# Kernel optimization log

Measured on AMD Instinct MI355X. Metric: run time of the kernel, lower is better.

## Reference

```python
import jax, jax.numpy as jnp
import numpy as np

N = 10000      # nodes
E = 320000     # edges (before self-loops)
IN_DIM = 128
HID = 64
OUT = 32
HEADS = 8
NEG_SLOPE = 0.2  # PyG GATConv default leaky_relu slope


def gat_conv(x, W, a_src, a_dst, b, src, dst, num_nodes, heads, d):
    """One PyG-style GATConv layer (eval mode, concat=True).
    x: [N, F_in], W: [F_in, heads*d], a_src/a_dst: [heads, d], b: [heads*d]
    src/dst: [E'] int edge endpoints (self-loops already included).
    """
    h = (x @ W).reshape(num_nodes, heads, d)              # [N, H, D]
    alpha_s = jnp.sum(h * a_src, axis=-1)                 # [N, H]
    alpha_d = jnp.sum(h * a_dst, axis=-1)                 # [N, H]
    logits = jax.nn.leaky_relu(alpha_s[src] + alpha_d[dst], NEG_SLOPE)  # [E', H]
    # segment softmax over incoming edges of each destination node
    m = jax.lax.stop_gradient(
        jax.ops.segment_max(logits, dst, num_segments=num_nodes))      # [N, H]
    e = jnp.exp(logits - m[dst])                          # [E', H]
    denom = jax.ops.segment_sum(e, dst, num_segments=num_nodes)        # [N, H]
    alpha = e / denom[dst]                                # [E', H]
    out = jax.ops.segment_sum(alpha[:, :, None] * h[src], dst,
                              num_segments=num_nodes)     # [N, H, D]
    return out.reshape(num_nodes, heads * d) + b


def setup_inputs() -> dict:
    key = jax.random.key(0)
    ks = jax.random.split(key, 10)
    x = jax.random.normal(ks[0], (N, IN_DIM), jnp.float32)
    edge_index = jax.random.randint(ks[1], (2, E), 0, N, dtype=jnp.int64)
    s1 = 1.0 / np.sqrt(IN_DIM)
    W1 = jax.random.normal(ks[2], (IN_DIM, HEADS * HID), jnp.float32) * s1
    a1_src = jax.random.normal(ks[3], (HEADS, HID), jnp.float32) * 0.1
    a1_dst = jax.random.normal(ks[4], (HEADS, HID), jnp.float32) * 0.1
    b1 = jnp.zeros((HEADS * HID,), jnp.float32)
    s2 = 1.0 / np.sqrt(HEADS * HID)
    W2 = jax.random.normal(ks[5], (HEADS * HID, OUT), jnp.float32) * s2
    a2_src = jax.random.normal(ks[6], (1, OUT), jnp.float32) * 0.1
    a2_dst = jax.random.normal(ks[7], (1, OUT), jnp.float32) * 0.1
    b2 = jnp.zeros((OUT,), jnp.float32)
    return {"x": x, "edge_index": edge_index,
            "W1": W1, "a1_src": a1_src, "a1_dst": a1_dst, "b1": b1,
            "W2": W2, "a2_src": a2_src, "a2_dst": a2_dst, "b2": b2}


def reference(x, edge_index, W1, a1_src, a1_dst, b1, W2, a2_src, a2_dst, b2):
    # add self-loops (PyG GATConv default add_self_loops=True)
    loops = jnp.arange(N, dtype=edge_index.dtype)
    src = jnp.concatenate([edge_index[0], loops])
    dst = jnp.concatenate([edge_index[1], loops])
    # dropout layers are identity in eval mode
    h = gat_conv(x, W1, a1_src, a1_dst, b1, src, dst, N, HEADS, HID)
    h = jax.nn.elu(h)
    out = gat_conv(h, W2, a2_src, a2_dst, b2, src, dst, N, 1, OUT)
    return out
```

## Files before the change

### kernel.cpp

```cpp
#include <hip/hip_runtime.h>
#include <math.h>

#define N_NODES 10000
#define E_EDGES 320000
#define EA      (E_EDGES + N_NODES)
#define IN_DIM  128
#define HID     512
#define HEADS   8
#define OUT_DIM 32
#define NEG     0.2f
#define CAP     160
#define CAPP    164
#define N_PAD   10048
#define NRB     628
#define RB_SH   4096

#define PWB  32
#define ZBK  40
#define SCB  645

typedef __attribute__((ext_vector_type(8))) short bf16x8;
typedef __attribute__((ext_vector_type(4))) float f32x4;

__device__ __forceinline__ float leaky(float x){ return x > 0.f ? x : NEG * x; }

__device__ __forceinline__ unsigned short bf16rn(float x){
    unsigned int b = __float_as_uint(x);
    b += 0x7fffu + ((b >> 16) & 1u);
    return (unsigned short)(b >> 16);
}

__device__ __forceinline__ unsigned short f16bits(float x){
    _Float16 h = (_Float16)x;
    return __builtin_bit_cast(unsigned short, h);
}

__device__ __forceinline__ float f16val(unsigned short u){
    return (float)__builtin_bit_cast(_Float16, u);
}

__global__ void k_pre(const float* __restrict__ x, const float* __restrict__ W1,
                      int* __restrict__ cnt,
                      unsigned short* __restrict__ Ax, unsigned short* __restrict__ Bt){
    int b = blockIdx.x, t = threadIdx.x;
    if (b < NRB){
        __shared__ float xs[16 * 132];
        int rb = b;
#pragma unroll
        for (int j = 0; j < 2; j++){
            int idx = t + j * 256;
            int r = idx >> 5, c4 = idx & 31;
            int row = rb * 16 + r;
            float4 v = make_float4(0.f, 0.f, 0.f, 0.f);
            if (row < N_NODES)
                v = *reinterpret_cast<const float4*>(x + (size_t)row * IN_DIM + c4 * 4);
            *reinterpret_cast<float4*>(&xs[r * 132 + c4 * 4]) = v;
        }
        __syncthreads();
        int l15 = t & 15, kk8 = t >> 4;
        unsigned short hi[8], lo[8];
#pragma unroll
        for (int el = 0; el < 8; el++){
            float f = xs[l15 * 132 + kk8 * 8 + el];
            hi[el] = bf16rn(f);
            lo[el] = bf16rn(f - __uint_as_float((unsigned)hi[el] << 16));
        }
        uint4 H, L;
        H.x = hi[0] | ((unsigned)hi[1] << 16); H.y = hi[2] | ((unsigned)hi[3] << 16);
        H.z = hi[4] | ((unsigned)hi[5] << 16); H.w = hi[6] | ((unsigned)hi[7] << 16);
        L.x = lo[0] | ((unsigned)lo[1] << 16); L.y = lo[2] | ((unsigned)lo[3] << 16);
        L.z = lo[4] | ((unsigned)lo[5] << 16); L.w = lo[6] | ((unsigned)lo[7] << 16);
        unsigned short* base = Ax + (size_t)rb * RB_SH;
        *reinterpret_cast<uint4*>(base + (kk8 * 16 + l15) * 8) = H;
        *reinterpret_cast<uint4*>(base + 2048 + (kk8 * 16 + l15) * 8) = L;
    } else if (b < NRB + PWB){
        __shared__ float wsh[128 * 17];
        int nb = b - NRB;
        int j = t & 15, kr = t >> 4;
#pragma unroll
        for (int it = 0; it < 8; it++){
            int k = it * 16 + kr;
            wsh[k * 17 + j] = W1[(size_t)k * HID + nb * 16 + j];
        }
        __syncthreads();
        int l15 = t & 15, kk8 = t >> 4;
        unsigned short hi[8], lo[8];
#pragma unroll
        for (int el = 0; el < 8; el++){
            float f = wsh[(kk8 * 8 + el) * 17 + l15];
            hi[el] = bf16rn(f);
            lo[el] = bf16rn(f - __uint_as_float((unsigned)hi[el] << 16));
        }
        uint4 H, L;
        H.x = hi[0] | ((unsigned)hi[1] << 16); H.y = hi[2] | ((unsigned)hi[3] << 16);
        H.z = hi[4] | ((unsigned)hi[5] << 16); H.w = hi[6] | ((unsigned)hi[7] << 16);
        L.x = lo[0] | ((unsigned)lo[1] << 16); L.y = lo[2] | ((unsigned)lo[3] << 16);
        L.z = lo[4] | ((unsigned)lo[5] << 16); L.w = lo[6] | ((unsigned)lo[7] << 16);
        unsigned short* base = Bt + (size_t)nb * RB_SH;
        *reinterpret_cast<uint4*>(base + (kk8 * 16 + l15) * 8) = H;
        *reinterpret_cast<uint4*>(base + 2048 + (kk8 * 16 + l15) * 8) = L;
    } else {
        int i = (b - NRB - PWB) * 256 + t;
        if (i < N_NODES) cnt[i] = 0;
    }
}

__launch_bounds__(512)
__global__ void k_sg(const int* __restrict__ eidx, int* __restrict__ cnt,
                     int* __restrict__ esrc,
                     const unsigned short* __restrict__ Ax,
                     const unsigned short* __restrict__ Bt,
                     const float* __restrict__ a1s, const float* __restrict__ a1d,
                     unsigned short* __restrict__ h1,
                     float* __restrict__ as1, float* __restrict__ ad1){
    if (blockIdx.x < SCB){
        int e = blockIdx.x * 512 + threadIdx.x;
        if (e < EA){
            int d, s;
            if (e < E_EDGES){ s = eidx[e]; d = eidx[E_EDGES + e]; }
            else { s = d = e - E_EDGES; }
            int pos = atomicAdd(&cnt[d], 1);
            if (pos < CAP) esrc[d * CAP + pos] = s;
        }
        return;
    }
    int rb = blockIdx.x - SCB;
    int by = threadIdx.x >> 6;
    int lane = threadIdx.x & 63;
    int l15 = lane & 15, grp = lane >> 4;
    int m0 = rb * 16;
    int n0 = by * 64;
    const unsigned short* ap = Ax + (size_t)rb * RB_SH + (size_t)lane * 8;
    bf16x8 a_hi[4], a_lo[4];
#pragma unroll
    for (int ks = 0; ks < 4; ks++){
        a_hi[ks] = *reinterpret_cast<const bf16x8*>(ap + ks * 512);
        a_lo[ks] = *reinterpret_cast<const bf16x8*>(ap + 2048 + ks * 512);
    }
    const unsigned short* bp = Bt + (size_t)(by * 4) * RB_SH + (size_t)lane * 8;
    f32x4 acc[4] = {};
#pragma unroll
    for (int ks = 0; ks < 4; ks++){
#pragma unroll
        for (int ns = 0; ns < 4; ns++){
            const unsigned short* bb = bp + (size_t)ns * RB_SH + ks * 512;
            bf16x8 b_hi = *reinterpret_cast<const bf16x8*>(bb);
            bf16x8 b_lo = *reinterpret_cast<const bf16x8*>(bb + 2048);
            acc[ns] = __builtin_amdgcn_mfma_f32_16x16x32_bf16(a_hi[ks], b_hi, acc[ns], 0, 0, 0);
            acc[ns] = __builtin_amdgcn_mfma_f32_16x16x32_bf16(a_lo[ks], b_hi, acc[ns], 0, 0, 0);
            acc[ns] = __builtin_amdgcn_mfma_f32_16x16x32_bf16(a_hi[ks], b_lo, acc[ns], 0, 0, 0);
        }
    }
    float vs[4] = {0.f, 0.f, 0.f, 0.f}, vd[4] = {0.f, 0.f, 0.f, 0.f};
#pragma unroll
    for (int ns = 0; ns < 4; ns++){
        int c = n0 + ns * 16 + l15;
        float a_s = a1s[c], a_d = a1d[c];
#pragma unroll
        for (int r = 0; r < 4; r++){
            float v = acc[ns][r];
            int rr = m0 + grp * 4 + r;
            if (rr < N_NODES) h1[(size_t)rr * HID + c] = f16bits(v);
            vs[r] += v * a_s; vd[r] += v * a_d;
        }
    }
#pragma unroll
    for (int r = 0; r < 4; r++){
#pragma unroll
        for (int off = 8; off >= 1; off >>= 1){
            vs[r] += __shfl_xor(vs[r], off);
            vd[r] += __shfl_xor(vd[r], off);
        }
    }
    if (l15 == 0){
#pragma unroll
        for (int r = 0; r < 4; r++){
            int rr = m0 + grp * 4 + r;
            if (rr < N_NODES){ as1[rr * HEADS + by] = vs[r]; ad1[rr * HEADS + by] = vd[r]; }
        }
    }
}

__launch_bounds__(128)
__global__ void k_agg1(const unsigned short* __restrict__ h1,
                       const float* __restrict__ as1, const float* __restrict__ ad1,
                       const int* __restrict__ cnt, const int* __restrict__ esrc,
                       const float* __restrict__ b1, float* __restrict__ h1b){
    int gp = blockIdx.x & 3;
    int ng = blockIdx.x >> 2;
    int t  = threadIdx.x;
    int sub = t >> 4;
    int tl  = t & 15;
    int n = ng * 8 + sub;
    int g0 = gp * 2, g1 = g0 + 1;
    int c = cnt[n]; if (c > CAP) c = CAP;
    int beg = n * CAP;
    __shared__ float s_w0[8][CAPP];
    __shared__ float s_w1[8][CAPP];
    __shared__ unsigned s_off[8][CAPP];
    float adn0 = ad1[(n << 3) + g0];
    float adn1 = ad1[(n << 3) + g1];
    float pm0 = -INFINITY, pm1 = -INFINITY;
    for (int i = tl; i < c; i += 16){
        int s = esrc[beg + i];
        float lg0 = leaky(as1[(s << 3) + g0] + adn0);
        float lg1 = leaky(as1[(s << 3) + g1] + adn1);
        s_w0[sub][i] = lg0; s_w1[sub][i] = lg1;
        s_off[sub][i] = (unsigned)s << 9;
        pm0 = fmaxf(pm0, lg0); pm1 = fmaxf(pm1, lg1);
    }
#pragma unroll
    for (int off = 8; off >= 1; off >>= 1){
        pm0 = fmaxf(pm0, __shfl_xor(pm0, off, 16));
        pm1 = fmaxf(pm1, __shfl_xor(pm1, off, 16));
    }
    __syncthreads();
    for (int i = tl; i < c; i += 16){
        s_w0[sub][i] = __expf(s_w0[sub][i] - pm0);
        s_w1[sub][i] = __expf(s_w1[sub][i] - pm1);
    }
    __syncthreads();
    unsigned dbase = (unsigned)(gp * 128 + tl * 8);
    const float* swp = (tl >= 8) ? &s_w1[sub][0] : &s_w0[sub][0];
    const unsigned* sop = &s_off[sub][0];
    float ac[4][8] = {};
    float dn[4] = {};
    int i = 0;
    for (; i + 3 < c; i += 4){
#pragma unroll
        for (int u = 0; u < 4; u++){
            float w = swp[i + u];
            uint4 hv = *reinterpret_cast<const uint4*>(h1 + sop[i + u] + dbase);
            ac[u][0] += w * f16val((unsigned short)(hv.x & 0xffffu));
            ac[u][1] += w * f16val((unsigned short)(hv.x >> 16));
            ac[u][2] += w * f16val((unsigned short)(hv.y & 0xffffu));
            ac[u][3] += w * f16val((unsigned short)(hv.y >> 16));
            ac[u][4] += w * f16val((unsigned short)(hv.z & 0xffffu));
            ac[u][5] += w * f16val((unsigned short)(hv.z >> 16));
            ac[u][6] += w * f16val((unsigned short)(hv.w & 0xffffu));
            ac[u][7] += w * f16val((unsigned short)(hv.w >> 16));
            dn[u] += w;
        }
    }
    for (; i < c; i++){
        float w = swp[i];
        uint4 hv = *reinterpret_cast<const uint4*>(h1 + sop[i] + dbase);
        ac[0][0] += w * f16val((unsigned short)(hv.x & 0xffffu));
        ac[0][1] += w * f16val((unsigned short)(hv.x >> 16));
        ac[0][2] += w * f16val((unsigned short)(hv.y & 0xffffu));
        ac[0][3] += w * f16val((unsigned short)(hv.y >> 16));
        ac[0][4] += w * f16val((unsigned short)(hv.z & 0xffffu));
        ac[0][5] += w * f16val((unsigned short)(hv.z >> 16));
        ac[0][6] += w * f16val((unsigned short)(hv.w & 0xffffu));
        ac[0][7] += w * f16val((unsigned short)(hv.w >> 16));
        dn[0] += w;
    }
    float den = (dn[0] + dn[1]) + (dn[2] + dn[3]);
    float rd = 1.f / den;
    float4 bv0 = *reinterpret_cast<const float4*>(b1 + dbase);
    float4 bv1 = *reinterpret_cast<const float4*>(b1 + dbase + 4);
    float o[8];
#pragma unroll
    for (int j = 0; j < 8; j++){
        float v = ((ac[0][j] + ac[1][j]) + (ac[2][j] + ac[3][j])) * rd;
        float bb = (j < 4) ? (&bv0.x)[j] : (&bv1.x)[j - 4];
        v += bb;
        o[j] = v > 0.f ? v : expm1f(v);
    }
    float4 o0, o1;
    o0.x = o[0]; o0.y = o[1]; o0.z = o[2]; o0.w = o[3];
    o1.x = o[4]; o1.y = o[5]; o1.z = o[6]; o1.w = o[7];
    *reinterpret_cast<float4*>(h1b + (size_t)n * HID + dbase) = o0;
    *reinterpret_cast<float4*>(h1b + (size_t)n * HID + dbase + 4) = o1;
}

__launch_bounds__(128)
__global__ void k_gemm2(const float* __restrict__ h1b, const float* __restrict__ W2,
                        const float* __restrict__ a2s, const float* __restrict__ a2d,
                        float* __restrict__ h2, float* __restrict__ as2,
                        float* __restrict__ ad2){
    __shared__ float hs[16 * 516];
    int t = threadIdx.x;
    int n0 = blockIdx.x * 16;
    const float4* src = reinterpret_cast<const float4*>(h1b + (size_t)n0 * HID);
    for (int i = t; i < 2048; i += 128){
        int r = i >> 7, c4 = i & 127;
        *reinterpret_cast<float4*>(&hs[r * 516 + c4 * 4]) = src[i];
    }
    __syncthreads();
    int nl = t >> 3, cg = t & 7, c0 = cg * 4;
    float a0 = 0.f, a1 = 0.f, a2 = 0.f, a3 = 0.f;
#pragma unroll 2
    for (int k4 = 0; k4 < 128; k4++){
        float4 hv = *reinterpret_cast<const float4*>(&hs[nl * 516 + k4 * 4]);
        float4 w0 = *reinterpret_cast<const float4*>(W2 + (k4 * 4 + 0) * OUT_DIM + c0);
        float4 w1 = *reinterpret_cast<const float4*>(W2 + (k4 * 4 + 1) * OUT_DIM + c0);
        float4 w2 = *reinterpret_cast<const float4*>(W2 + (k4 * 4 + 2) * OUT_DIM + c0);
        float4 w3 = *reinterpret_cast<const float4*>(W2 + (k4 * 4 + 3) * OUT_DIM + c0);
        a0 += hv.x * w0.x + hv.y * w1.x + hv.z * w2.x + hv.w * w3.x;
        a1 += hv.x * w0.y + hv.y * w1.y + hv.z * w2.y + hv.w * w3.y;
        a2 += hv.x * w0.z + hv.y * w1.z + hv.z * w2.z + hv.w * w3.z;
        a3 += hv.x * w0.w + hv.y * w1.w + hv.z * w2.w + hv.w * w3.w;
    }
    float4 o; o.x = a0; o.y = a1; o.z = a2; o.w = a3;
    *reinterpret_cast<float4*>(h2 + (size_t)(n0 + nl) * OUT_DIM + c0) = o;
    float4 s4 = *reinterpret_cast<const float4*>(a2s + c0);
    float4 d4 = *reinterpret_cast<const float4*>(a2d + c0);
    float vs = a0 * s4.x + a1 * s4.y + a2 * s4.z + a3 * s4.w;
    float vd = a0 * d4.x + a1 * d4.y + a2 * d4.z + a3 * d4.w;
#pragma unroll
    for (int off = 4; off >= 1; off >>= 1){
        vs += __shfl_xor(vs, off);
        vd += __shfl_xor(vd, off);
    }
    if (cg == 0){ as2[n0 + nl] = vs; ad2[n0 + nl] = vd; }
}

__launch_bounds__(256)
__global__ void k_agg2(const float* __restrict__ h2, const float* __restrict__ as2,
                       const float* __restrict__ ad2, const int* __restrict__ cnt,
                       const int* __restrict__ esrc,
                       const float* __restrict__ b2, float* __restrict__ out){
    int wv = threadIdx.x >> 6;
    int lane = threadIdx.x & 63;
    int n = blockIdx.x * 4 + wv;
    __shared__ float    s_w[4][CAPP];
    __shared__ unsigned s_off[4][CAPP];
    int c = cnt[n]; if (c > CAP) c = CAP;
    int beg = n * CAP;
    float adn = ad2[n];
    float pm = -INFINITY;
    for (int i = lane; i < c; i += 64){
        int s = esrc[beg + i];
        float lg = leaky(as2[s] + adn);
        s_off[wv][i] = (unsigned)s * OUT_DIM;
        s_w[wv][i] = lg;
        pm = fmaxf(pm, lg);
    }
#pragma unroll
    for (int off = 32; off >= 1; off >>= 1)
        pm = fmaxf(pm, __shfl_xor(pm, off));
    __syncthreads();
    for (int i = lane; i < c; i += 64) s_w[wv][i] = __expf(s_w[wv][i] - pm);
    __syncthreads();
    int eslot = lane >> 3, dgrp = lane & 7, d0 = dgrp * 4;
    float4 acc = make_float4(0.f, 0.f, 0.f, 0.f);
    float den = 0.f;
    for (int i = eslot; i < c; i += 8){
        float w = s_w[wv][i];
        float4 hv = *reinterpret_cast<const float4*>(h2 + s_off[wv][i] + d0);
        acc.x += w * hv.x; acc.y += w * hv.y;
        acc.z += w * hv.z; acc.w += w * hv.w;
        den += w;
    }
#pragma unroll
    for (int off = 8; off <= 32; off <<= 1){
        acc.x += __shfl_xor(acc.x, off);
        acc.y += __shfl_xor(acc.y, off);
        acc.z += __shfl_xor(acc.z, off);
        acc.w += __shfl_xor(acc.w, off);
        den   += __shfl_xor(den, off);
    }
    if (eslot == 0){
        float rd = 1.f / den;
        float4 bv = *reinterpret_cast<const float4*>(b2 + d0);
        float4 o;
        o.x = acc.x * rd + bv.x; o.y = acc.y * rd + bv.y;
        o.z = acc.z * rd + bv.z; o.w = acc.w * rd + bv.w;
        *reinterpret_cast<float4*>(out + (size_t)n * OUT_DIM + d0) = o;
    }
}

extern "C" void kernel_launch(void* const* d_in, const int* in_sizes, int n_in,
                              void* d_out, int out_size, void* d_ws, size_t ws_size,
                              hipStream_t stream){
    const float* x   = (const float*)d_in[0];
    const int*  eidx = (const int*)  d_in[1];
    const float* W1  = (const float*)d_in[2];
    const float* a1s = (const float*)d_in[3];
    const float* a1d = (const float*)d_in[4];
    const float* b1  = (const float*)d_in[5];
    const float* W2  = (const float*)d_in[6];
    const float* a2s = (const float*)d_in[7];
    const float* a2d = (const float*)d_in[8];
    const float* b2  = (const float*)d_in[9];
    float* out = (float*)d_out;

    char* ws = (char*)d_ws;
    size_t off = 0;
    auto alloc = [&](size_t bytes) -> void* {
        void* p = ws + off;
        off += (bytes + 255) & ~(size_t)255;
        return p;
    };
    unsigned short* h1 = (unsigned short*)alloc((size_t)N_NODES * HID * 2);
    float* h1b  = (float*)alloc((size_t)N_NODES * HID * 4);
    unsigned short* Bt = (unsigned short*)alloc((size_t)32 * RB_SH * 2);
    float* as1  = (float*)alloc((size_t)N_NODES * HEADS * 4);
    float* ad1  = (float*)alloc((size_t)N_NODES * HEADS * 4);
    float* h2   = (float*)alloc((size_t)N_NODES * OUT_DIM * 4);
    float* vs2  = (float*)alloc((size_t)N_NODES * 4);
    float* vd2  = (float*)alloc((size_t)N_NODES * 4);
    int* cnt    = (int*)alloc((size_t)N_NODES * 4);
    int* esrc   = (int*)alloc((size_t)N_NODES * CAP * 4);
    unsigned short* Ax = (unsigned short*)h1b;

    k_pre <<<NRB + PWB + ZBK, 256, 0, stream>>>(x, W1, cnt, Ax, Bt);
    k_sg  <<<SCB + NRB, 512, 0, stream>>>(eidx, cnt, esrc, Ax, Bt, a1s, a1d,
                                          h1, as1, ad1);
    k_agg1<<<(N_NODES / 8) * 4, 128, 0, stream>>>(h1, as1, ad1, cnt, esrc, b1, h1b);
    k_gemm2<<<N_NODES / 16, 128, 0, stream>>>(h1b, W2, a2s, a2d, h2, vs2, vd2);
    k_agg2<<<N_NODES / 4, 256, 0, stream>>>(h2, vs2, vd2, cnt, esrc, b2, out);
}
```

Measured before the change: 109.5 us.

## Fuse x bf16 split into GEMM1 kernel and widen agg1 to two edge lanes

Moves the hi/lo bf16 splitting of x from the pre-pass into the GEMM1 blocks, which now stage x rows in shared memory and build the MFMA A fragments in registers. This drops the round trip of writing and re-reading the Ax staging buffer. Separately, k_agg1 now uses 32 threads per node, with two halves processing alternating edges and combining via shuffles, to raise memory-level parallelism in the gather. The costs are the split arithmetic repeated in each of the 8 waves per block and half the agg1 threads sitting idle during the final write.

After: 111.0 us. About the same (+1.3%).

```diff
diff --git a/kernel.cpp b/kernel.cpp
--- a/kernel.cpp
+++ b/kernel.cpp
@@ -11,7 +11,6 @@
 #define NEG     0.2f
 #define CAP     160
 #define CAPP    164
-#define N_PAD   10048
 #define NRB     628
 #define RB_SH   4096
 
@@ -39,43 +38,12 @@
     return (float)__builtin_bit_cast(_Float16, u);
 }
 
-__global__ void k_pre(const float* __restrict__ x, const float* __restrict__ W1,
-                      int* __restrict__ cnt,
-                      unsigned short* __restrict__ Ax, unsigned short* __restrict__ Bt){
+__global__ void k_pre(const float* __restrict__ W1, int* __restrict__ cnt,
+                      unsigned short* __restrict__ Bt){
     int b = blockIdx.x, t = threadIdx.x;
-    if (b < NRB){
-        __shared__ float xs[16 * 132];
-        int rb = b;
-#pragma unroll
-        for (int j = 0; j < 2; j++){
-            int idx = t + j * 256;
-            int r = idx >> 5, c4 = idx & 31;
-            int row = rb * 16 + r;
-            float4 v = make_float4(0.f, 0.f, 0.f, 0.f);
-            if (row < N_NODES)
-                v = *reinterpret_cast<const float4*>(x + (size_t)row * IN_DIM + c4 * 4);
-            *reinterpret_cast<float4*>(&xs[r * 132 + c4 * 4]) = v;
-        }
-        __syncthreads();
-        int l15 = t & 15, kk8 = t >> 4;
-        unsigned short hi[8], lo[8];
-#pragma unroll
-        for (int el = 0; el < 8; el++){
-            float f = xs[l15 * 132 + kk8 * 8 + el];
-            hi[el] = bf16rn(f);
-            lo[el] = bf16rn(f - __uint_as_float((unsigned)hi[el] << 16));
-        }
-        uint4 H, L;
-        H.x = hi[0] | ((unsigned)hi[1] << 16); H.y = hi[2] | ((unsigned)hi[3] << 16);
-        H.z = hi[4] | ((unsigned)hi[5] << 16); H.w = hi[6] | ((unsigned)hi[7] << 16);
-        L.x = lo[0] | ((unsigned)lo[1] << 16); L.y = lo[2] | ((unsigned)lo[3] << 16);
-        L.z = lo[4] | ((unsigned)lo[5] << 16); L.w = lo[6] | ((unsigned)lo[7] << 16);
-        unsigned short* base = Ax + (size_t)rb * RB_SH;
-        *reinterpret_cast<uint4*>(base + (kk8 * 16 + l15) * 8) = H;
-        *reinterpret_cast<uint4*>(base + 2048 + (kk8 * 16 + l15) * 8) = L;
-    } else if (b < NRB + PWB){
+    if (b < PWB){
         __shared__ float wsh[128 * 17];
-        int nb = b - NRB;
+        int nb = b;
         int j = t & 15, kr = t >> 4;
 #pragma unroll
         for (int it = 0; it < 8; it++){
@@ -100,7 +68,7 @@
         *reinterpret_cast<uint4*>(base + (kk8 * 16 + l15) * 8) = H;
         *reinterpret_cast<uint4*>(base + 2048 + (kk8 * 16 + l15) * 8) = L;
     } else {
-        int i = (b - NRB - PWB) * 256 + t;
+        int i = (b - PWB) * 256 + t;
         if (i < N_NODES) cnt[i] = 0;
     }
 }
@@ -108,11 +76,12 @@
 __launch_bounds__(512)
 __global__ void k_sg(const int* __restrict__ eidx, int* __restrict__ cnt,
                      int* __restrict__ esrc,
-                     const unsigned short* __restrict__ Ax,
+                     const float* __restrict__ x,
                      const unsigned short* __restrict__ Bt,
                      const float* __restrict__ a1s, const float* __restrict__ a1d,
                      unsigned short* __restrict__ h1,
                      float* __restrict__ as1, float* __restrict__ ad1){
+    __shared__ float xs[16 * 132];
     if (blockIdx.x < SCB){
         int e = blockIdx.x * 512 + threadIdx.x;
         if (e < EA){
@@ -125,17 +94,34 @@
         return;
     }
     int rb = blockIdx.x - SCB;
-    int by = threadIdx.x >> 6;
-    int lane = threadIdx.x & 63;
+    int t = threadIdx.x;
+    {
+        int r = t >> 5, c4 = t & 31;
+        int row = rb * 16 + r;
+        float4 v = make_float4(0.f, 0.f, 0.f, 0.f);
+        if (row < N_NODES)
+            v = *reinterpret_cast<const float4*>(x + (size_t)row * IN_DIM + c4 * 4);
+        *reinterpret_cast<float4*>(&xs[r * 132 + c4 * 4]) = v;
+    }
+    __syncthreads();
+    int by = t >> 6;
+    int lane = t & 63;
     int l15 = lane & 15, grp = lane >> 4;
     int m0 = rb * 16;
     int n0 = by * 64;
-    const unsigned short* ap = Ax + (size_t)rb * RB_SH + (size_t)lane * 8;
     bf16x8 a_hi[4], a_lo[4];
 #pragma unroll
     for (int ks = 0; ks < 4; ks++){
-        a_hi[ks] = *reinterpret_cast<const bf16x8*>(ap + ks * 512);
-        a_lo[ks] = *reinterpret_cast<const bf16x8*>(ap + 2048 + ks * 512);
+        short hs[8], ls[8];
+#pragma unroll
+        for (int el = 0; el < 8; el++){
+            float f = xs[l15 * 132 + ks * 32 + grp * 8 + el];
+            unsigned short h = bf16rn(f);
+            hs[el] = (short)h;
+            ls[el] = (short)bf16rn(f - __uint_as_float((unsigned)h << 16));
+        }
+        a_hi[ks] = *reinterpret_cast<bf16x8*>(hs);
+        a_lo[ks] = *reinterpret_cast<bf16x8*>(ls);
     }
     const unsigned short* bp = Bt + (size_t)(by * 4) * RB_SH + (size_t)lane * 8;
     f32x4 acc[4] = {};
@@ -181,7 +167,7 @@
     }
 }
 
-__launch_bounds__(128)
+__launch_bounds__(256)
 __global__ void k_agg1(const unsigned short* __restrict__ h1,
                        const float* __restrict__ as1, const float* __restrict__ ad1,
                        const int* __restrict__ cnt, const int* __restrict__ esrc,
@@ -189,8 +175,10 @@
     int gp = blockIdx.x & 3;
     int ng = blockIdx.x >> 2;
     int t  = threadIdx.x;
-    int sub = t >> 4;
-    int tl  = t & 15;
+    int sub = t >> 5;
+    int tl  = t & 31;
+    int l16 = tl & 15;
+    int half = tl >> 4;
     int n = ng * 8 + sub;
     int g0 = gp * 2, g1 = g0 + 1;
     int c = cnt[n]; if (c > CAP) c = CAP;
@@ -201,7 +189,7 @@
     float adn0 = ad1[(n << 3) + g0];
     float adn1 = ad1[(n << 3) + g1];
     float pm0 = -INFINITY, pm1 = -INFINITY;
-    for (int i = tl; i < c; i += 16){
+    for (int i = tl; i < c; i += 32){
         int s = esrc[beg + i];
         float lg0 = leaky(as1[(s << 3) + g0] + adn0);
         float lg1 = leaky(as1[(s << 3) + g1] + adn1);
@@ -210,27 +198,28 @@
         pm0 = fmaxf(pm0, lg0); pm1 = fmaxf(pm1, lg1);
     }
 #pragma unroll
-    for (int off = 8; off >= 1; off >>= 1){
-        pm0 = fmaxf(pm0, __shfl_xor(pm0, off, 16));
-        pm1 = fmaxf(pm1, __shfl_xor(pm1, off, 16));
-    }
-    __syncthreads();
-    for (int i = tl; i < c; i += 16){
+    for (int off = 16; off >= 1; off >>= 1){
+        pm0 = fmaxf(pm0, __shfl_xor(pm0, off));
+        pm1 = fmaxf(pm1, __shfl_xor(pm1, off));
+    }
+    __syncthreads();
+    for (int i = tl; i < c; i += 32){
         s_w0[sub][i] = __expf(s_w0[sub][i] - pm0);
         s_w1[sub][i] = __expf(s_w1[sub][i] - pm1);
     }
     __syncthreads();
-    unsigned dbase = (unsigned)(gp * 128 + tl * 8);
-    const float* swp = (tl >= 8) ? &s_w1[sub][0] : &s_w0[sub][0];
+    unsigned dbase = (unsigned)(gp * 128 + l16 * 8);
+    const float* swp = (l16 >= 8) ? &s_w1[sub][0] : &s_w0[sub][0];
     const unsigned* sop = &s_off[sub][0];
     float ac[4][8] = {};
     float dn[4] = {};
-    int i = 0;
-    for (; i + 3 < c; i += 4){
+    int i = half;
+    for (; i + 6 < c; i += 8){
 #pragma unroll
         for (int u = 0; u < 4; u++){
-            float w = swp[i + u];
-            uint4 hv = *reinterpret_cast<const uint4*>(h1 + sop[i + u] + dbase);
+            int idx = i + 2 * u;
+            float w = swp[idx];
+            uint4 hv = *reinterpret_cast<const uint4*>(h1 + sop[idx] + dbase);
             ac[u][0] += w * f16val((unsigned short)(hv.x & 0xffffu));
             ac[u][1] += w * f16val((unsigned short)(hv.x >> 16));
             ac[u][2] += w * f16val((unsigned short)(hv.y & 0xffffu));
@@ -242,7 +231,7 @@
             dn[u] += w;
         }
     }
-    for (; i < c; i++){
+    for (; i < c; i += 2){
         float w = swp[i];
         uint4 hv = *reinterpret_cast<const uint4*>(h1 + sop[i] + dbase);
         ac[0][0] += w * f16val((unsigned short)(hv.x & 0xffffu));
@@ -256,22 +245,32 @@
         dn[0] += w;
     }
     float den = (dn[0] + dn[1]) + (dn[2] + dn[3]);
-    float rd = 1.f / den;
-    float4 bv0 = *reinterpret_cast<const float4*>(b1 + dbase);
-    float4 bv1 = *reinterpret_cast<const float4*>(b1 + dbase + 4);
-    float o[8];
+    den += __shfl_xor(den, 16);
+    float accj[8];
 #pragma unroll
     for (int j = 0; j < 8; j++){
-        float v = ((ac[0][j] + ac[1][j]) + (ac[2][j] + ac[3][j])) * rd;
-        float bb = (j < 4) ? (&bv0.x)[j] : (&bv1.x)[j - 4];
-        v += bb;
-        o[j] = v > 0.f ? v : expm1f(v);
-    }
-    float4 o0, o1;
-    o0.x = o[0]; o0.y = o[1]; o0.z = o[2]; o0.w = o[3];
-    o1.x = o[4]; o1.y = o[5]; o1.z = o[6]; o1.w = o[7];
-    *reinterpret_cast<float4*>(h1b + (size_t)n * HID + dbase) = o0;
-    *reinterpret_cast<float4*>(h1b + (size_t)n * HID + dbase + 4) = o1;
+        float v = ((ac[0][j] + ac[1][j]) + (ac[2][j] + ac[3][j]));
+        v += __shfl_xor(v, 16);
+        accj[j] = v;
+    }
+    if (half == 0){
+        float rd = 1.f / den;
+        float4 bv0 = *reinterpret_cast<const float4*>(b1 + dbase);
+        float4 bv1 = *reinterpret_cast<const float4*>(b1 + dbase + 4);
+        float o[8];
+#pragma unroll
+        for (int j = 0; j < 8; j++){
+            float v = accj[j] * rd;
+            float bb = (j < 4) ? (&bv0.x)[j] : (&bv1.x)[j - 4];
+            v += bb;
+            o[j] = v > 0.f ? v : expm1f(v);
+        }
+        float4 o0, o1;
+        o0.x = o[0]; o0.y = o[1]; o0.z = o[2]; o0.w = o[3];
+        o1.x = o[4]; o1.y = o[5]; o1.z = o[6]; o1.w = o[7];
+        *reinterpret_cast<float4*>(h1b + (size_t)n * HID + dbase) = o0;
+        *reinterpret_cast<float4*>(h1b + (size_t)n * HID + dbase + 4) = o1;
+    }
 }
 
 __launch_bounds__(128)
@@ -403,12 +402,11 @@
     float* vd2  = (float*)alloc((size_t)N_NODES * 4);
     int* cnt    = (int*)alloc((size_t)N_NODES * 4);
     int* esrc   = (int*)alloc((size_t)N_NODES * CAP * 4);
-    unsigned short* Ax = (unsigned short*)h1b;
-
-    k_pre <<<NRB + PWB + ZBK, 256, 0, stream>>>(x, W1, cnt, Ax, Bt);
-    k_sg  <<<SCB + NRB, 512, 0, stream>>>(eidx, cnt, esrc, Ax, Bt, a1s, a1d,
+
+    k_pre <<<PWB + ZBK, 256, 0, stream>>>(W1, cnt, Bt);
+    k_sg  <<<SCB + NRB, 512, 0, stream>>>(eidx, cnt, esrc, x, Bt, a1s, a1d,
                                           h1, as1, ad1);
-    k_agg1<<<(N_NODES / 8) * 4, 128, 0, stream>>>(h1, as1, ad1, cnt, esrc, b1, h1b);
+    k_agg1<<<(N_NODES / 8) * 4, 256, 0, stream>>>(h1, as1, ad1, cnt, esrc, b1, h1b);
     k_gemm2<<<N_NODES / 16, 128, 0, stream>>>(h1b, W2, a2s, a2d, h2, vs2, vd2);
     k_agg2<<<N_NODES / 4, 256, 0, stream>>>(h2, vs2, vd2, cnt, esrc, b2, out);
 }
```
